# Optimization experiments

Hardware: AMD Instinct MI355X
Metric: run time of the kernel (lower is better)

Reference implementation:

```python
import jax, jax.numpy as jnp
import numpy as np

DIM = 768
H = 12
HD = DIM // H
SCALE = HD ** (-0.5)


def setup_inputs() -> dict:
    key = jax.random.key(0)
    ks = jax.random.split(key, 10)
    s = DIM ** (-0.5)
    x = jax.random.normal(ks[0], (8, 1024, DIM), dtype=jnp.float32)
    Wq = jax.random.normal(ks[1], (DIM, DIM), dtype=jnp.float32) * s
    Wk = jax.random.normal(ks[2], (DIM, DIM), dtype=jnp.float32) * s
    Wv = jax.random.normal(ks[3], (DIM, DIM), dtype=jnp.float32) * s
    Wl = jax.random.normal(ks[4], (H, H), dtype=jnp.float32) * (H ** -0.5)
    bl = jax.random.normal(ks[5], (H,), dtype=jnp.float32) * 0.02
    Ww = jax.random.normal(ks[6], (H, H), dtype=jnp.float32) * (H ** -0.5)
    bw = jax.random.normal(ks[7], (H,), dtype=jnp.float32) * 0.02
    Wp = jax.random.normal(ks[8], (DIM, DIM), dtype=jnp.float32) * s
    bp = jax.random.normal(ks[9], (DIM,), dtype=jnp.float32) * 0.02
    return {"x": x, "Wq": Wq, "Wk": Wk, "Wv": Wv, "Wl": Wl, "bl": bl,
            "Ww": Ww, "bw": bw, "Wp": Wp, "bp": bp}


def reference(x, Wq, Wk, Wv, Wl, bl, Ww, bw, Wp, bp):
    B, N, C = x.shape
    # QKV projections (no bias), split heads -> (B, H, N, hd)
    q = (x @ Wq).reshape(B, N, H, HD).transpose(0, 2, 1, 3) * SCALE
    k = (x @ Wk).reshape(B, N, H, HD).transpose(0, 2, 1, 3)
    v = (x @ Wv).reshape(B, N, H, HD).transpose(0, 2, 1, 3)
    # scores: (B, H, N, N)
    attn = jnp.einsum('bhid,bhjd->bhij', q, k)
    # talking heads pre-softmax: mix over head axis (Linear on last dim of BNNH)
    attn = jnp.einsum('bhij,gh->bgij', attn, Wl) + bl[None, :, None, None]
    attn = jax.nn.softmax(attn, axis=-1)
    # talking heads post-softmax
    attn = jnp.einsum('bhij,gh->bgij', attn, Ww) + bw[None, :, None, None]
    out = jnp.einsum('bhij,bhjd->bhid', attn, v)  # (B, H, N, hd)
    out = out.transpose(0, 2, 1, 3).reshape(B, N, C)
    return out @ Wp + bp
```

## Files before the change

kernel.cpp:

```cpp
#include <hip/hip_runtime.h>
#include <hip/hip_bf16.h>

#define DIM 768
#define NH 12
#define HD 64
#define SEQ 1024
#define BATCH 8
#define LOG2E 1.44269504f

typedef __bf16 bf16x8 __attribute__((ext_vector_type(8)));
typedef _Float16 f16x4 __attribute__((ext_vector_type(4)));
typedef float f32x4 __attribute__((ext_vector_type(4)));

__device__ __forceinline__ void gload_lds16(const __bf16* g, __bf16* l) {
  __builtin_amdgcn_global_load_lds(
      (const __attribute__((address_space(1))) void*)g,
      (__attribute__((address_space(3))) void*)l, 16, 0, 0);
}

__global__ __launch_bounds__(256) void xcvt(
    const float* __restrict__ X, __bf16* __restrict__ Xb)
{
  const size_t i = ((size_t)blockIdx.x * 256 + threadIdx.x) * 8;
  float4 a0 = *(const float4*)(X + i);
  float4 a1 = *(const float4*)(X + i + 4);
  bf16x8 v = { (__bf16)a0.x, (__bf16)a0.y, (__bf16)a0.z, (__bf16)a0.w,
               (__bf16)a1.x, (__bf16)a1.y, (__bf16)a1.z, (__bf16)a1.w };
  *(bf16x8*)(Xb + i) = v;
}

__global__ __launch_bounds__(256) void wtrans(
    const float* __restrict__ Wq, const float* __restrict__ Wk,
    const float* __restrict__ Wv, const float* __restrict__ Wp,
    __bf16* __restrict__ Tq, __bf16* __restrict__ Tk,
    __bf16* __restrict__ Tv, __bf16* __restrict__ Tp)
{
  const int z = blockIdx.z;
  const float* W = (z==0) ? Wq : (z==1) ? Wk : (z==2) ? Wv : Wp;
  __bf16* T = (z==0) ? Tq : (z==1) ? Tk : (z==2) ? Tv : Tp;
  __shared__ float tile[32][33];
  const int t = threadIdx.x, tx = t & 31, ty = t >> 5;
  const int k0 = blockIdx.y * 32, n0 = blockIdx.x * 32;
#pragma unroll
  for (int u = 0; u < 4; ++u)
    tile[ty + u*8][tx] = W[(size_t)(k0 + ty + u*8) * DIM + n0 + tx];
  __syncthreads();
#pragma unroll
  for (int u = 0; u < 4; ++u)
    T[(size_t)(n0 + ty + u*8) * DIM + k0 + tx] = (__bf16)tile[tx][ty + u*8];
}

__global__ __launch_bounds__(256) void gemm_qkv(
    const __bf16* __restrict__ Xb, const __bf16* __restrict__ WT,
    __bf16* __restrict__ Qo, __bf16* __restrict__ Ko, _Float16* __restrict__ Vt2)
{
  __shared__ __bf16 As[128 * 32];
  __shared__ __bf16 Bs[128 * 32];

  const int t = threadIdx.x, lane = t & 63, w = t >> 6;
  const int n16 = lane & 15, q = lane >> 4;
  const int m0 = blockIdx.y * 128, n0 = blockIdx.x * 128;
  const int wm = (w >> 1) * 64, wn = (w & 1) * 64;

  const int srow = t >> 2, scol = (t & 3) * 8;
  const __bf16* Ag = Xb + (size_t)(m0 + srow) * DIM + scol;
  const __bf16* Bg = WT + (size_t)(n0 + srow) * DIM + scol;
  __bf16* AsW0 = &As[w * 512];
  __bf16* AsW1 = &As[2048 + w * 512];
  __bf16* BsW0 = &Bs[w * 512];
  __bf16* BsW1 = &Bs[2048 + w * 512];

  f32x4 acc[4][4];
#pragma unroll
  for (int mt = 0; mt < 4; ++mt)
#pragma unroll
    for (int nt = 0; nt < 4; ++nt) acc[mt][nt] = (f32x4){0.f,0.f,0.f,0.f};

  for (int kb = 0; kb < DIM; kb += 32) {
    __syncthreads();
    gload_lds16(Ag + kb, AsW0);
    gload_lds16(Ag + (size_t)64 * DIM + kb, AsW1);
    gload_lds16(Bg + kb, BsW0);
    gload_lds16(Bg + (size_t)64 * DIM + kb, BsW1);
    __syncthreads();

    bf16x8 af[4], bg[4];
#pragma unroll
    for (int mt = 0; mt < 4; ++mt)
      af[mt] = *(const bf16x8*)&As[(wm + mt*16 + n16) * 32 + q*8];
#pragma unroll
    for (int nt = 0; nt < 4; ++nt)
      bg[nt] = *(const bf16x8*)&Bs[(wn + nt*16 + n16) * 32 + q*8];
#pragma unroll
    for (int mt = 0; mt < 4; ++mt)
#pragma unroll
      for (int nt = 0; nt < 4; ++nt)
        acc[mt][nt] = __builtin_amdgcn_mfma_f32_16x16x32_bf16(af[mt], bg[nt], acc[mt][nt], 0, 0, 0);
  }

#pragma unroll
  for (int nt = 0; nt < 4; ++nt) {
    const int n = n0 + wn + nt*16 + n16;
    const int z = n / DIM, c = n % DIM;
    const int h = c >> 6, d = c & 63;
#pragma unroll
    for (int mt = 0; mt < 4; ++mt) {
#pragma unroll
      for (int r = 0; r < 4; ++r) {
        const int row = m0 + wm + mt*16 + q*4 + r;
        const int bb = row >> 10, ii = row & 1023;
        const float v = acc[mt][nt][r];
        if (z == 0)
          Qo[(((size_t)bb*NH + h)*SEQ + ii)*HD + d] = (__bf16)(v * 0.125f);
        else if (z == 1)
          Ko[(((size_t)bb*NH + h)*SEQ + ii)*HD + d] = (__bf16)v;
        else
          Vt2[((((size_t)bb*NH + h)*64 + (ii >> 4))*HD + d)*16 + (ii & 15)] = (_Float16)v;
      }
    }
  }
}

__global__ __launch_bounds__(256, 2) void attn_fused(
    const __bf16* __restrict__ Qg, const __bf16* __restrict__ Kg,
    const _Float16* __restrict__ Vt2,
    const float* __restrict__ Wl, const float* __restrict__ bl,
    const float* __restrict__ Ww, const float* __restrict__ bw,
    __bf16* __restrict__ Aout)
{
  __shared__ _Float16 Sl[2][12][324];
  __shared__ _Float16 Pl[2][16 * 248];
  __shared__ float Wls[144];
  __shared__ float blS[12];
  __shared__ float Lx[4][12][16];

  const int t = threadIdx.x, lane = t & 63, w = t >> 6;
  const int n16 = lane & 15, q = lane >> 4;
  const int h0 = w * 3;
  const int b = blockIdx.x, i0 = blockIdx.y * 16;
  const size_t bbase = (size_t)b * NH * SEQ * HD;

  if (t < 144) Wls[t] = Wl[t] * LOG2E;
  if (t < 12)  blS[t] = bl[t] * LOG2E;

  f16x4 wlA, wwA;
  f32x4 blC, bwC;
#pragma unroll
  for (int j = 0; j < 4; ++j) {
    const int k = q*4 + j;
    wlA[j] = (n16 < 12 && k < 12) ? (_Float16)(Wl[n16*12 + k] * LOG2E) : (_Float16)0.f;
    wwA[j] = (n16 < 12 && k < 12) ? (_Float16)Ww[n16*12 + k] : (_Float16)0.f;
    blC[j] = (k < 12) ? bl[k] * LOG2E : 0.f;
    bwC[j] = (k < 12) ? bw[k] : 0.f;
  }

  const f32x4 z4 = {0.f, 0.f, 0.f, 0.f};
  __syncthreads();

  bf16x8 qA0[12], qA1[12];
#pragma unroll
  for (int h = 0; h < 12; ++h) {
    const __bf16* qp = Qg + bbase + ((size_t)h*SEQ + i0 + n16)*HD + q*8;
    qA0[h] = *(const bf16x8*)qp;
    qA1[h] = *(const bf16x8*)(qp + 32);
  }

  float lsum[12];
#pragma unroll
  for (int g = 0; g < 12; ++g) lsum[g] = 0.f;

  for (int tt = 0; tt < 16; ++tt) {
    const int jt = tt*4 + w;
    f32x4 sh[12];
#pragma unroll
    for (int h = 0; h < 12; ++h) {
      const __bf16* kp = Kg + bbase + ((size_t)h*SEQ + jt*16 + n16)*HD + q*8;
      bf16x8 k0 = *(const bf16x8*)kp;
      bf16x8 k1 = *(const bf16x8*)(kp + 32);
      f32x4 s = __builtin_amdgcn_mfma_f32_16x16x32_bf16(k0, qA0[h], z4, 0, 0, 0);
      sh[h] = __builtin_amdgcn_mfma_f32_16x16x32_bf16(k1, qA1[h], s, 0, 0, 0);
    }
#pragma unroll
    for (int g = 0; g < 12; ++g) {
      const f32x4 wr0 = *(const f32x4*)&Wls[g*12];
      const f32x4 wr1 = *(const f32x4*)&Wls[g*12 + 4];
      const f32x4 wr2 = *(const f32x4*)&Wls[g*12 + 8];
      f32x4 a = { blS[g], blS[g], blS[g], blS[g] };
#pragma unroll
      for (int h = 0; h < 4; ++h)
#pragma unroll
        for (int r = 0; r < 4; ++r) a[r] += wr0[h] * sh[h][r];
#pragma unroll
      for (int h = 0; h < 4; ++h)
#pragma unroll
        for (int r = 0; r < 4; ++r) a[r] += wr1[h] * sh[4+h][r];
#pragma unroll
      for (int h = 0; h < 4; ++h)
#pragma unroll
        for (int r = 0; r < 4; ++r) a[r] += wr2[h] * sh[8+h][r];
      lsum[g] += __builtin_amdgcn_exp2f(a[0]) + __builtin_amdgcn_exp2f(a[1])
               + __builtin_amdgcn_exp2f(a[2]) + __builtin_amdgcn_exp2f(a[3]);
    }
  }

#pragma unroll
  for (int g = 0; g < 12; ++g) {
    float l = lsum[g];
    l += __shfl_xor(l, 16);
    l += __shfl_xor(l, 32);
    lsum[g] = l;
  }
  if (lane < 16) {
#pragma unroll
    for (int g = 0; g < 12; ++g) Lx[w][g][lane] = lsum[g];
  }
  __syncthreads();

  float linv[4][4];
#pragma unroll
  for (int c = 0; c < 4; ++c)
#pragma unroll
    for (int r = 0; r < 4; ++r) {
      const int g = q*4 + r;
      if (g < 12) {
        const int i = w*4 + c;
        float l = Lx[0][g][i] + Lx[1][g][i] + Lx[2][g][i] + Lx[3][g][i];
        linv[c][r] = 1.0f / l;
      } else {
        linv[c][r] = 0.f;
      }
    }

  bf16x8 qf[3][2];
#pragma unroll
  for (int hh = 0; hh < 3; ++hh)
#pragma unroll
    for (int cc = 0; cc < 2; ++cc)
      qf[hh][cc] = *(const bf16x8*)(Qg + bbase + ((size_t)(h0+hh)*SEQ + i0 + n16)*HD + cc*32 + q*8);

  f32x4 oacc[3][4];
#pragma unroll
  for (int hh = 0; hh < 3; ++hh)
#pragma unroll
    for (int dc = 0; dc < 4; ++dc) oacc[hh][dc] = z4;

  bf16x8 kC[3][2], kN[3][2];
  f16x4 vC[3][4], vN[3][4];
#pragma unroll
  for (int hh = 0; hh < 3; ++hh) {
    const __bf16* kp = Kg + bbase + ((size_t)(h0+hh)*SEQ + n16)*HD + q*8;
    kC[hh][0] = *(const bf16x8*)kp;
    kC[hh][1] = *(const bf16x8*)(kp + 32);
  }

#pragma unroll 2
  for (int jt = 0; jt < SEQ/16; ++jt) {
    const int buf = jt & 1;
    const int jn = (jt < SEQ/16 - 1) ? jt + 1 : jt;
#pragma unroll
    for (int hh = 0; hh < 3; ++hh) {
      const __bf16* kp = Kg + bbase + ((size_t)(h0+hh)*SEQ + jn*16 + n16)*HD + q*8;
      kN[hh][0] = *(const bf16x8*)kp;
      kN[hh][1] = *(const bf16x8*)(kp + 32);
    }
#pragma unroll
    for (int hh = 0; hh < 3; ++hh) {
      const _Float16* vb = Vt2 + (((size_t)(b*NH + h0 + hh)*64 + jt)*HD)*16;
#pragma unroll
      for (int dc = 0; dc < 4; ++dc)
        vN[hh][dc] = *(const f16x4*)(vb + (size_t)(dc*16 + n16)*16 + q*4);
    }
    __builtin_amdgcn_s_setprio(1);
#pragma unroll
    for (int hh = 0; hh < 3; ++hh) {
      f32x4 s = __builtin_amdgcn_mfma_f32_16x16x32_bf16(kC[hh][0], qf[hh][0], z4, 0, 0, 0);
      s = __builtin_amdgcn_mfma_f32_16x16x32_bf16(kC[hh][1], qf[hh][1], s, 0, 0, 0);
      f16x4 sh2 = { (_Float16)s[0], (_Float16)s[1], (_Float16)s[2], (_Float16)s[3] };
      *(f16x4*)&Sl[buf][h0+hh][n16*20 + q*4] = sh2;
    }
    __builtin_amdgcn_s_setprio(0);
    __syncthreads();
    if (jt > 0) {
      f16x4 pa[3];
#pragma unroll
      for (int hh = 0; hh < 3; ++hh)
        pa[hh] = *(const f16x4*)&Pl[1 - buf][n16*248 + (h0+hh)*20 + q*4];
      __builtin_amdgcn_s_setprio(1);
#pragma unroll
      for (int hh = 0; hh < 3; ++hh)
#pragma unroll
        for (int dc = 0; dc < 4; ++dc)
          oacc[hh][dc] = __builtin_amdgcn_mfma_f32_16x16x16f16(pa[hh], vC[hh][dc], oacc[hh][dc], 0, 0, 0);
      __builtin_amdgcn_s_setprio(0);
    }
#pragma unroll
    for (int c = 0; c < 4; ++c) {
      const int i = w*4 + c;
      f16x4 sf;
#pragma unroll
      for (int dd = 0; dd < 4; ++dd) {
        int h = q*4 + dd; if (h > 11) h = 11;
        sf[dd] = Sl[buf][h][i*20 + n16];
      }
      f32x4 sm = __builtin_amdgcn_mfma_f32_16x16x16f16(wlA, sf, blC, 0, 0, 0);
      f16x4 pnf;
#pragma unroll
      for (int r = 0; r < 4; ++r)
        pnf[r] = (_Float16)(__builtin_amdgcn_exp2f(sm[r]) * linv[c][r]);
      f32x4 p2 = __builtin_amdgcn_mfma_f32_16x16x16f16(wwA, pnf, bwC, 0, 0, 0);
      if (q < 3) {
#pragma unroll
        for (int r = 0; r < 4; ++r)
          Pl[buf][i*248 + (q*4 + r)*20 + n16] = (_Float16)p2[r];
      }
    }
#pragma unroll
    for (int hh = 0; hh < 3; ++hh) {
      kC[hh][0] = kN[hh][0]; kC[hh][1] = kN[hh][1];
#pragma unroll
      for (int dc = 0; dc < 4; ++dc) vC[hh][dc] = vN[hh][dc];
    }
  }
  __syncthreads();
#pragma unroll
  for (int hh = 0; hh < 3; ++hh) {
    const int g2 = h0 + hh;
    f16x4 pa = *(const f16x4*)&Pl[1][n16*248 + g2*20 + q*4];
#pragma unroll
    for (int dc = 0; dc < 4; ++dc)
      oacc[hh][dc] = __builtin_amdgcn_mfma_f32_16x16x16f16(pa, vC[hh][dc], oacc[hh][dc], 0, 0, 0);
  }

#pragma unroll
  for (int hh = 0; hh < 3; ++hh)
#pragma unroll
    for (int dc = 0; dc < 4; ++dc)
#pragma unroll
      for (int r = 0; r < 4; ++r)
        Aout[((size_t)(b*SEQ + i0 + q*4 + r))*DIM + (h0+hh)*HD + dc*16 + n16] =
            (__bf16)oacc[hh][dc][r];
}

__global__ __launch_bounds__(256) void gemm_proj(
    const __bf16* __restrict__ A, const __bf16* __restrict__ WpT,
    const float* __restrict__ bp, float* __restrict__ Out)
{
  __shared__ __bf16 As[128 * 32];
  __shared__ __bf16 Bs[128 * 32];

  const int t = threadIdx.x, lane = t & 63, w = t >> 6;
  const int n16 = lane & 15, q = lane >> 4;
  const int m0 = blockIdx.y * 128, n0 = blockIdx.x * 128;
  const int wm = (w >> 1) * 64, wn = (w & 1) * 64;

  const int srow = t >> 2, scol = (t & 3) * 8;
  const __bf16* Ag = A + (size_t)(m0 + srow) * DIM + scol;
  const __bf16* Bg = WpT + (size_t)(n0 + srow) * DIM + scol;
  __bf16* AsW0 = &As[w * 512];
  __bf16* AsW1 = &As[2048 + w * 512];
  __bf16* BsW0 = &Bs[w * 512];
  __bf16* BsW1 = &Bs[2048 + w * 512];

  f32x4 acc[4][4];
#pragma unroll
  for (int nt = 0; nt < 4; ++nt) {
    const float bpv = bp[n0 + wn + nt*16 + n16];
#pragma unroll
    for (int mt = 0; mt < 4; ++mt)
#pragma unroll
      for (int r = 0; r < 4; ++r) acc[mt][nt][r] = bpv;
  }

  for (int kb = 0; kb < DIM; kb += 32) {
    __syncthreads();
    gload_lds16(Ag + kb, AsW0);
    gload_lds16(Ag + (size_t)64 * DIM + kb, AsW1);
    gload_lds16(Bg + kb, BsW0);
    gload_lds16(Bg + (size_t)64 * DIM + kb, BsW1);
    __syncthreads();

    bf16x8 af[4], bg[4];
#pragma unroll
    for (int mt = 0; mt < 4; ++mt)
      af[mt] = *(const bf16x8*)&As[(wm + mt*16 + n16) * 32 + q*8];
#pragma unroll
    for (int nt = 0; nt < 4; ++nt)
      bg[nt] = *(const bf16x8*)&Bs[(wn + nt*16 + n16) * 32 + q*8];
#pragma unroll
    for (int mt = 0; mt < 4; ++mt)
#pragma unroll
      for (int nt = 0; nt < 4; ++nt)
        acc[mt][nt] = __builtin_amdgcn_mfma_f32_16x16x32_bf16(af[mt], bg[nt], acc[mt][nt], 0, 0, 0);
  }

#pragma unroll
  for (int nt = 0; nt < 4; ++nt) {
    const int n = n0 + wn + nt*16 + n16;
#pragma unroll
    for (int mt = 0; mt < 4; ++mt)
#pragma unroll
      for (int r = 0; r < 4; ++r) {
        const int row = m0 + wm + mt*16 + q*4 + r;
        Out[(size_t)row * DIM + n] = acc[mt][nt][r];
      }
  }
}

extern "C" void kernel_launch(void* const* d_in, const int* in_sizes, int n_in,
                              void* d_out, int out_size, void* d_ws, size_t ws_size,
                              hipStream_t stream) {
  const float* x  = (const float*)d_in[0];
  const float* Wq = (const float*)d_in[1];
  const float* Wk = (const float*)d_in[2];
  const float* Wv = (const float*)d_in[3];
  const float* Wl = (const float*)d_in[4];
  const float* bl = (const float*)d_in[5];
  const float* Ww = (const float*)d_in[6];
  const float* bw = (const float*)d_in[7];
  const float* Wp = (const float*)d_in[8];
  const float* bp = (const float*)d_in[9];

  char* p = (char*)d_ws;
  const size_t WSZ = (size_t)DIM * DIM * 2;
  const size_t TSZ = (size_t)BATCH * NH * SEQ * HD * 2;
  __bf16*   WqT = (__bf16*)p;            p += WSZ;
  __bf16*   WkT = (__bf16*)p;            p += WSZ;
  __bf16*   WvT = (__bf16*)p;            p += WSZ;
  __bf16*   WpT = (__bf16*)p;            p += WSZ;
  __bf16*   Q   = (__bf16*)p;            p += TSZ;
  __bf16*   K   = (__bf16*)p;            p += TSZ;
  _Float16* V2  = (_Float16*)p;          p += TSZ;
  __bf16*   AO  = (__bf16*)p;            p += TSZ;
  __bf16*   Xb  = (__bf16*)p;            p += TSZ;

  xcvt<<<dim3((BATCH*SEQ*DIM)/(256*8)), 256, 0, stream>>>(x, Xb);
  wtrans<<<dim3(24, 24, 4), 256, 0, stream>>>(Wq, Wk, Wv, Wp, WqT, WkT, WvT, WpT);
  gemm_qkv<<<dim3(18, 64), 256, 0, stream>>>(Xb, WqT, Q, K, V2);
  attn_fused<<<dim3(BATCH, SEQ/16), 256, 0, stream>>>(Q, K, V2, Wl, bl, Ww, bw, AO);
  gemm_proj<<<dim3(6, 64), 256, 0, stream>>>(AO, WpT, bp, (float*)d_out);
}
```

Baseline: 524.4 us.

## Stream Q per head and mix heads incrementally in softmax-denominator pass

The first attention pass no longer keeps all 12 heads of Q fragments (24 bf16x8 vectors) in registers. It reloads Q per head inside the key-tile loop and folds each head's score straight into 12 mixed accumulators, using a transposed copy of Wl in LDS. The pre-softmax bias is taken out of the exponent and applied once as an exp2(bl) factor on the denominator. The aim is to cut VGPR pressure and per-tile live state, in exchange for repeated Q loads from cache on every key tile.

```diff
diff --git a/kernel.cpp b/kernel.cpp
--- a/kernel.cpp
+++ b/kernel.cpp
@@ -130,7 +130,7 @@
 {
   __shared__ _Float16 Sl[2][12][324];
   __shared__ _Float16 Pl[2][16 * 248];
-  __shared__ float Wls[144];
+  __shared__ float WlsT[144];
   __shared__ float blS[12];
   __shared__ float Lx[4][12][16];
 
@@ -140,7 +140,7 @@
   const int b = blockIdx.x, i0 = blockIdx.y * 16;
   const size_t bbase = (size_t)b * NH * SEQ * HD;
 
-  if (t < 144) Wls[t] = Wl[t] * LOG2E;
+  if (t < 144) WlsT[(t % 12) * 12 + (t / 12)] = Wl[t] * LOG2E;
   if (t < 12)  blS[t] = bl[t] * LOG2E;
 
   f16x4 wlA, wwA;
@@ -157,50 +157,49 @@
   const f32x4 z4 = {0.f, 0.f, 0.f, 0.f};
   __syncthreads();
 
-  bf16x8 qA0[12], qA1[12];
-#pragma unroll
-  for (int h = 0; h < 12; ++h) {
-    const __bf16* qp = Qg + bbase + ((size_t)h*SEQ + i0 + n16)*HD + q*8;
-    qA0[h] = *(const bf16x8*)qp;
-    qA1[h] = *(const bf16x8*)(qp + 32);
-  }
-
   float lsum[12];
 #pragma unroll
   for (int g = 0; g < 12; ++g) lsum[g] = 0.f;
 
+  const __bf16* kbase = Kg + bbase + ((size_t)(w*16) + n16)*HD + q*8;
+  const __bf16* qbase = Qg + bbase + ((size_t)(i0 + n16))*HD + q*8;
+
   for (int tt = 0; tt < 16; ++tt) {
-    const int jt = tt*4 + w;
-    f32x4 sh[12];
+    f32x4 a[12];
+#pragma unroll
+    for (int g = 0; g < 12; ++g) a[g] = z4;
+    const __bf16* kp = kbase + (size_t)tt * 64 * HD;
+    const __bf16* qp = qbase;
 #pragma unroll
     for (int h = 0; h < 12; ++h) {
-      const __bf16* kp = Kg + bbase + ((size_t)h*SEQ + jt*16 + n16)*HD + q*8;
       bf16x8 k0 = *(const bf16x8*)kp;
       bf16x8 k1 = *(const bf16x8*)(kp + 32);
-      f32x4 s = __builtin_amdgcn_mfma_f32_16x16x32_bf16(k0, qA0[h], z4, 0, 0, 0);
-      sh[h] = __builtin_amdgcn_mfma_f32_16x16x32_bf16(k1, qA1[h], s, 0, 0, 0);
-    }
-#pragma unroll
-    for (int g = 0; g < 12; ++g) {
-      const f32x4 wr0 = *(const f32x4*)&Wls[g*12];
-      const f32x4 wr1 = *(const f32x4*)&Wls[g*12 + 4];
-      const f32x4 wr2 = *(const f32x4*)&Wls[g*12 + 8];
-      f32x4 a = { blS[g], blS[g], blS[g], blS[g] };
-#pragma unroll
-      for (int h = 0; h < 4; ++h)
-#pragma unroll
-        for (int r = 0; r < 4; ++r) a[r] += wr0[h] * sh[h][r];
-#pragma unroll
-      for (int h = 0; h < 4; ++h)
-#pragma unroll
-        for (int r = 0; r < 4; ++r) a[r] += wr1[h] * sh[4+h][r];
-#pragma unroll
-      for (int h = 0; h < 4; ++h)
-#pragma unroll
-        for (int r = 0; r < 4; ++r) a[r] += wr2[h] * sh[8+h][r];
-      lsum[g] += __builtin_amdgcn_exp2f(a[0]) + __builtin_amdgcn_exp2f(a[1])
-               + __builtin_amdgcn_exp2f(a[2]) + __builtin_amdgcn_exp2f(a[3]);
-    }
+      bf16x8 q0 = *(const bf16x8*)qp;
+      bf16x8 q1 = *(const bf16x8*)(qp + 32);
+      kp += (size_t)SEQ * HD;
+      qp += (size_t)SEQ * HD;
+      f32x4 s = __builtin_amdgcn_mfma_f32_16x16x32_bf16(k0, q0, z4, 0, 0, 0);
+      s = __builtin_amdgcn_mfma_f32_16x16x32_bf16(k1, q1, s, 0, 0, 0);
+      const f32x4 w0 = *(const f32x4*)&WlsT[h*12];
+      const f32x4 w1 = *(const f32x4*)&WlsT[h*12 + 4];
+      const f32x4 w2 = *(const f32x4*)&WlsT[h*12 + 8];
+#pragma unroll
+      for (int g = 0; g < 4; ++g)
+#pragma unroll
+        for (int r = 0; r < 4; ++r) a[g][r] += w0[g] * s[r];
+#pragma unroll
+      for (int g = 0; g < 4; ++g)
+#pragma unroll
+        for (int r = 0; r < 4; ++r) a[4+g][r] += w1[g] * s[r];
+#pragma unroll
+      for (int g = 0; g < 4; ++g)
+#pragma unroll
+        for (int r = 0; r < 4; ++r) a[8+g][r] += w2[g] * s[r];
+    }
+#pragma unroll
+    for (int g = 0; g < 12; ++g)
+      lsum[g] += __builtin_amdgcn_exp2f(a[g][0]) + __builtin_amdgcn_exp2f(a[g][1])
+               + __builtin_amdgcn_exp2f(a[g][2]) + __builtin_amdgcn_exp2f(a[g][3]);
   }
 
 #pragma unroll
@@ -225,7 +224,7 @@
       if (g < 12) {
         const int i = w*4 + c;
         float l = Lx[0][g][i] + Lx[1][g][i] + Lx[2][g][i] + Lx[3][g][i];
-        linv[c][r] = 1.0f / l;
+        linv[c][r] = 1.0f / (l * __builtin_amdgcn_exp2f(blS[g]));
       } else {
         linv[c][r] = 0.f;
       }
```

After: 526.9 us. No clear change (+0.5%).
